# Kernel tuning notes

Measured on AMD Instinct MI355X. Metric: run time of the kernel, lower is better.

## Reference

```python
import jax, jax.numpy as jnp
import numpy as np

EPS_FEAT = 1e-4   # stabilizer eps inside favorp_projection
EPS_DEN = 0.01    # clamp_min eps for the attention denominator


def favorp_projection(data, projection_matrix, is_query):
    # data: [b, h, n, d]; projection_matrix: [h, m, d]
    d = data.shape[-1]
    data_normalizer = d ** (-0.25)
    ratio = projection_matrix.shape[1] ** (-0.5)
    data_dash = jnp.einsum('bhnd,hmd->bhnm', data_normalizer * data, projection_matrix)
    diag_data = (jnp.sum(data * data, axis=-1) * 0.5 * data_normalizer * data_normalizer)[..., None]
    if is_query:
        stabilizer = jax.lax.stop_gradient(jnp.max(data_dash, axis=-1, keepdims=True))
    else:
        stabilizer = jax.lax.stop_gradient(jnp.max(data_dash, axis=(-1, -2), keepdims=True))
    return ratio * jnp.exp(data_dash - diag_data - stabilizer) + EPS_FEAT


def setup_inputs() -> dict:
    key = jax.random.key(0)
    ks = jax.random.split(key, 12)
    N, B, E, H, D, M = 4096, 4, 1024, 16, 64, 64
    s = E ** -0.5
    return {
        'query': jax.random.normal(ks[0], (N, B, E), jnp.float32),
        'key': jax.random.normal(ks[1], (N, B, E), jnp.float32),
        'value': jax.random.normal(ks[2], (N, B, E), jnp.float32),
        'Wq': jax.random.normal(ks[3], (E, E), jnp.float32) * s,
        'bq': jax.random.normal(ks[4], (E,), jnp.float32) * 0.02,
        'Wk': jax.random.normal(ks[5], (E, E), jnp.float32) * s,
        'bk': jax.random.normal(ks[6], (E,), jnp.float32) * 0.02,
        'Wv': jax.random.normal(ks[7], (E, E), jnp.float32) * s,
        'bv': jax.random.normal(ks[8], (E,), jnp.float32) * 0.02,
        'Wo': jax.random.normal(ks[9], (E, E), jnp.float32) * s,
        'bo': jax.random.normal(ks[10], (E,), jnp.float32) * 0.02,
        'proj': jax.random.normal(ks[11], (H, M, D), jnp.float32),
    }


def reference(query, key, value, Wq, bq, Wk, bk, Wv, bv, Wo, bo, proj):
    H = proj.shape[0]
    # [n, b, e] -> [b, n, e]
    q_in = query.transpose(1, 0, 2)
    k_in = key.transpose(1, 0, 2)
    v_in = value.transpose(1, 0, 2)
    B, N, E = q_in.shape
    D = E // H

    def lin(x, W, b):
        return jnp.einsum('bne,fe->bnf', x, W) + b

    def split_heads(x):  # [b, n, e] -> [b, h, n, d]
        return x.reshape(B, N, H, D).transpose(0, 2, 1, 3)

    q = split_heads(lin(q_in, Wq, bq))
    k = split_heads(lin(k_in, Wk, bk))
    v = split_heads(lin(v_in, Wv, bv))

    q_prime = favorp_projection(q, proj, is_query=True)   # [b, h, n, m]
    k_prime = favorp_projection(k, proj, is_query=False)  # [b, h, n, m]

    # non-causal linear attention: O(n * m * d)
    kv = jnp.einsum('bhnm,bhnd->bhmd', k_prime, v)
    qkv = jnp.einsum('bhnm,bhmd->bhnd', q_prime, kv)
    normalizer = jnp.einsum('bhnm,bhm->bhn', q_prime, k_prime.sum(axis=2))
    output = qkv / jnp.maximum(normalizer[..., None], EPS_DEN)

    attn_output = output.transpose(0, 2, 1, 3).reshape(B, N, E)  # b h n d -> b n (h d)
    out = lin(attn_output, Wo, bo)
    return out.transpose(1, 0, 2)  # back to [n, b, e]
```

## Files before the change

### kernel.cpp

```cpp
#include <hip/hip_runtime.h>
#include <math.h>

#define B_   4
#define N_   4096
#define E_   1024
#define H_   16
#define BN_  (B_*N_)
#define BH_  (B_*H_)
#define SPLITK 8

#define NRM_C   0.35355339059327373f
#define DIAG_C  0.0625f
#define RATIO_C 0.125f
#define EPSF    1e-4f
#define EPSD    0.01f

typedef __attribute__((ext_vector_type(8))) short bf16x8;
typedef __attribute__((ext_vector_type(4))) float f32x4;

__device__ __forceinline__ unsigned short f32_to_bf16(float x) {
    unsigned int u = __float_as_uint(x);
    unsigned int r = (u + 0x7fffu + ((u >> 16) & 1u)) >> 16;
    return (unsigned short)r;
}
__device__ __forceinline__ float bf16_to_f32(unsigned short h) {
    return __uint_as_float(((unsigned int)h) << 16);
}

__device__ __forceinline__ unsigned int pk_bf16(float a, float b) {
    unsigned int r;
    asm("v_cvt_pk_bf16_f32 %0, %1, %2" : "=v"(r) : "v"(a), "v"(b));
    return r;
}

__device__ __forceinline__ void f32x8_split(float4 fa, float4 fb, bf16x8& hi, bf16x8& lo) {
    unsigned int h0 = pk_bf16(fa.x, fa.y), h1 = pk_bf16(fa.z, fa.w);
    unsigned int h2 = pk_bf16(fb.x, fb.y), h3 = pk_bf16(fb.z, fb.w);
    float e0 = __uint_as_float(h0 << 16), e1 = __uint_as_float(h0 & 0xffff0000u);
    float e2 = __uint_as_float(h1 << 16), e3 = __uint_as_float(h1 & 0xffff0000u);
    float e4 = __uint_as_float(h2 << 16), e5 = __uint_as_float(h2 & 0xffff0000u);
    float e6 = __uint_as_float(h3 << 16), e7 = __uint_as_float(h3 & 0xffff0000u);
    unsigned int l0 = pk_bf16(fa.x - e0, fa.y - e1), l1 = pk_bf16(fa.z - e2, fa.w - e3);
    unsigned int l2 = pk_bf16(fb.x - e4, fb.y - e5), l3 = pk_bf16(fb.z - e6, fb.w - e7);
    union { unsigned int u[4]; bf16x8 v; } H, L;
    H.u[0] = h0; H.u[1] = h1; H.u[2] = h2; H.u[3] = h3;
    L.u[0] = l0; L.u[1] = l1; L.u[2] = l2; L.u[3] = l3;
    hi = H.v; lo = L.v;
}

__device__ __forceinline__ void atomicMaxF(float* addr, float v) {
    if (v >= 0.f) atomicMax((int*)addr, __float_as_int(v));
    else          atomicMin((unsigned int*)addr, __float_as_uint(v));
}

__global__ void init_stab(float* stab) {
    if (threadIdx.x < BH_) stab[threadIdx.x] = -INFINITY;
}

template<int IN_MODE>
__global__ __launch_bounds__(256) void convert_split(const float* __restrict__ src,
                                                     unsigned short* __restrict__ hi,
                                                     unsigned short* __restrict__ lo,
                                                     int total4)
{
    int i = blockIdx.x * 256 + threadIdx.x;
    const int stride = gridDim.x * 256;
    for (; i < total4; i += stride) {
        long e4 = (long)i * 4;
        const float* p;
        if (IN_MODE == 0) {
            long r = e4 >> 10; int e = (int)(e4 & 1023);
            int b = (int)(r >> 12), n = (int)(r & 4095);
            p = src + (((long)(n * B_ + b)) << 10) + e;
        } else {
            p = src + e4;
        }
        float4 v = *(const float4*)p;
        ushort4 h, l;
        h.x = f32_to_bf16(v.x); l.x = f32_to_bf16(v.x - bf16_to_f32(h.x));
        h.y = f32_to_bf16(v.y); l.y = f32_to_bf16(v.y - bf16_to_f32(h.y));
        h.z = f32_to_bf16(v.z); l.z = f32_to_bf16(v.z - bf16_to_f32(h.z));
        h.w = f32_to_bf16(v.w); l.w = f32_to_bf16(v.w - bf16_to_f32(h.w));
        *(ushort4*)(hi + e4) = h;
        *(ushort4*)(lo + e4) = l;
    }
}

__device__ __forceinline__ void gl_lds16(const unsigned short* g, unsigned short* l) {
    __builtin_amdgcn_global_load_lds((const __attribute__((address_space(1))) void*)g,
                                     (__attribute__((address_space(3))) void*)l, 16, 0, 0);
}

#define SMEM_DYN8 147456

template<int MODE>
__global__ __launch_bounds__(512, 2) void gemm8p(const unsigned short* __restrict__ Ahi,
                                                 const unsigned short* __restrict__ Alo,
                                                 const unsigned short* __restrict__ Bhi,
                                                 const unsigned short* __restrict__ Blo,
                                                 const float* __restrict__ bias,
                                                 float* __restrict__ Y)
{
    extern __shared__ char SMEM8[];
    unsigned short* U = (unsigned short*)SMEM8;
    const int t = threadIdx.x;
    const int w = t >> 6, lane = t & 63;
    const int row0 = blockIdx.x * 256, col0 = blockIdx.y * 128;
    const int wrow = (w >> 1) * 64, wcol = (w & 1) * 64;
    const int g = lane >> 4, rl = lane & 15;

    int gi0 = t, gi1 = 512 + t;
    int ar0 = gi0 >> 2, as0 = gi0 & 3;
    int ar1 = gi1 >> 2, as1 = gi1 & 3;
    const long aSrc0 = (long)(row0 + ar0) * E_ + ((as0 ^ (ar0 & 3)) << 3);
    const long aSrc1 = (long)(row0 + ar1) * E_ + ((as1 ^ (ar1 & 3)) << 3);
    const int aDst0 = (w * 64) * 8;
    const int aDst1 = (512 + w * 64) * 8;
    const long bSrc = (long)(col0 + (t >> 2)) * E_ + (((t & 3) ^ ((t >> 2) & 3)) << 3);
    const int bDst = (w * 64) * 8;

    f32x4 acc[4][4];
#pragma unroll
    for (int m = 0; m < 4; ++m)
#pragma unroll
        for (int n = 0; n < 4; ++n) acc[m][n] = (f32x4){0.f, 0.f, 0.f, 0.f};

#define STAGE_FULL(TILE, BUFI) {                                        \
        const int k0_ = (TILE) * 32;                                    \
        unsigned short* bu_ = U + (BUFI) * 24576;                       \
        gl_lds16(Ahi + aSrc0 + k0_, bu_ + aDst0);                       \
        gl_lds16(Ahi + aSrc1 + k0_, bu_ + aDst1);                       \
        gl_lds16(Alo + aSrc0 + k0_, bu_ + 8192 + aDst0);                \
        gl_lds16(Alo + aSrc1 + k0_, bu_ + 8192 + aDst1);                \
        gl_lds16(Bhi + bSrc + k0_, bu_ + 16384 + bDst);                 \
        gl_lds16(Blo + bSrc + k0_, bu_ + 20480 + bDst); }

    STAGE_FULL(0, 0);
    STAGE_FULL(1, 1);
    asm volatile("s_waitcnt vmcnt(6)" ::: "memory");
    __builtin_amdgcn_s_barrier();
    __builtin_amdgcn_sched_barrier(0);

    for (int tt = 0; tt < 32; ++tt) {
        const unsigned short* sb = U + (tt % 3) * 24576;
        unsigned short* ub = U + ((tt + 2) % 3) * 24576;
        const bool st = (tt + 2 < 32);
        const int k2 = (tt + 2) * 32;
        bf16x8 bhf[4], blf[4];

#pragma unroll
        for (int n = 0; n < 4; ++n) {
            int r = wcol + n * 16 + rl;
            int off = r * 32 + ((g ^ (r & 3)) << 3);
            bhf[n] = *(const bf16x8*)(sb + 16384 + off);
            blf[n] = *(const bf16x8*)(sb + 20480 + off);
        }
        {
            int r = wrow + rl;
            int off = r * 32 + ((g ^ (r & 3)) << 3);
            bf16x8 ah = *(const bf16x8*)(sb + off);
            bf16x8 al = *(const bf16x8*)(sb + 8192 + off);
            if (st) { gl_lds16(Ahi + aSrc0 + k2, ub + aDst0);
                      gl_lds16(Ahi + aSrc1 + k2, ub + aDst1); }
            asm volatile("s_waitcnt lgkmcnt(0)" ::: "memory");
            __builtin_amdgcn_sched_barrier(0);
            __builtin_amdgcn_s_setprio(1);
#pragma unroll
            for (int n = 0; n < 4; ++n)
                acc[0][n] = __builtin_amdgcn_mfma_f32_16x16x32_bf16(ah, bhf[n], acc[0][n], 0, 0, 0);
#pragma unroll
            for (int n = 0; n < 4; ++n)
                acc[0][n] = __builtin_amdgcn_mfma_f32_16x16x32_bf16(ah, blf[n], acc[0][n], 0, 0, 0);
#pragma unroll
            for (int n = 0; n < 4; ++n)
                acc[0][n] = __builtin_amdgcn_mfma_f32_16x16x32_bf16(al, bhf[n], acc[0][n], 0, 0, 0);
            __builtin_amdgcn_s_setprio(0);
        }
        __builtin_amdgcn_s_barrier();
        __builtin_amdgcn_sched_barrier(0);

        {
            int r = wrow + 16 + rl;
            int off = r * 32 + ((g ^ (r & 3)) << 3);
            bf16x8 ah = *(const bf16x8*)(sb + off);
            bf16x8 al = *(const bf16x8*)(sb + 8192 + off);
            if (st) { gl_lds16(Alo + aSrc0 + k2, ub + 8192 + aDst0);
                      gl_lds16(Alo + aSrc1 + k2, ub + 8192 + aDst1); }
            asm volatile("s_waitcnt lgkmcnt(0)" ::: "memory");
            __builtin_amdgcn_sched_barrier(0);
            __builtin_amdgcn_s_setprio(1);
#pragma unroll
            for (int n = 0; n < 4; ++n)
                acc[1][n] = __builtin_amdgcn_mfma_f32_16x16x32_bf16(ah, bhf[n], acc[1][n], 0, 0, 0);
#pragma unroll
            for (int n = 0; n < 4; ++n)
                acc[1][n] = __builtin_amdgcn_mfma_f32_16x16x32_bf16(ah, blf[n], acc[1][n], 0, 0, 0);
#pragma unroll
            for (int n = 0; n < 4; ++n)
                acc[1][n] = __builtin_amdgcn_mfma_f32_16x16x32_bf16(al, bhf[n], acc[1][n], 0, 0, 0);
            __builtin_amdgcn_s_setprio(0);
        }
        __builtin_amdgcn_s_barrier();
        __builtin_amdgcn_sched_barrier(0);

        {
            int r = wrow + 32 + rl;
            int off = r * 32 + ((g ^ (r & 3)) << 3);
            bf16x8 ah = *(const bf16x8*)(sb + off);
            bf16x8 al = *(const bf16x8*)(sb + 8192 + off);
            if (st) gl_lds16(Bhi + bSrc + k2, ub + 16384 + bDst);
            asm volatile("s_waitcnt lgkmcnt(0)" ::: "memory");
            __builtin_amdgcn_sched_barrier(0);
            __builtin_amdgcn_s_setprio(1);
#pragma unroll
            for (int n = 0; n < 4; ++n)
                acc[2][n] = __builtin_amdgcn_mfma_f32_16x16x32_bf16(ah, bhf[n], acc[2][n], 0, 0, 0);
#pragma unroll
            for (int n = 0; n < 4; ++n)
                acc[2][n] = __builtin_amdgcn_mfma_f32_16x16x32_bf16(ah, blf[n], acc[2][n], 0, 0, 0);
#pragma unroll
            for (int n = 0; n < 4; ++n)
                acc[2][n] = __builtin_amdgcn_mfma_f32_16x16x32_bf16(al, bhf[n], acc[2][n], 0, 0, 0);
            __builtin_amdgcn_s_setprio(0);
        }
        __builtin_amdgcn_s_barrier();
        __builtin_amdgcn_sched_barrier(0);

        {
            int r = wrow + 48 + rl;
            int off = r * 32 + ((g ^ (r & 3)) << 3);
            bf16x8 ah = *(const bf16x8*)(sb + off);
            bf16x8 al = *(const bf16x8*)(sb + 8192 + off);
            if (st) gl_lds16(Blo + bSrc + k2, ub + 20480 + bDst);
            asm volatile("s_waitcnt lgkmcnt(0)" ::: "memory");
            __builtin_amdgcn_sched_barrier(0);
            __builtin_amdgcn_s_setprio(1);
#pragma unroll
            for (int n = 0; n < 4; ++n)
                acc[3][n] = __builtin_amdgcn_mfma_f32_16x16x32_bf16(ah, bhf[n], acc[3][n], 0, 0, 0);
#pragma unroll
            for (int n = 0; n < 4; ++n)
                acc[3][n] = __builtin_amdgcn_mfma_f32_16x16x32_bf16(ah, blf[n], acc[3][n], 0, 0, 0);
#pragma unroll
            for (int n = 0; n < 4; ++n)
                acc[3][n] = __builtin_amdgcn_mfma_f32_16x16x32_bf16(al, bhf[n], acc[3][n], 0, 0, 0);
            __builtin_amdgcn_s_setprio(0);
        }
        if (tt < 31) {
            if (st) asm volatile("s_waitcnt vmcnt(6)" ::: "memory");
            else    asm volatile("s_waitcnt vmcnt(0)" ::: "memory");
            __builtin_amdgcn_s_barrier();
            __builtin_amdgcn_sched_barrier(0);
        }
    }
#undef STAGE_FULL

    float bv[4];
#pragma unroll
    for (int n = 0; n < 4; ++n) bv[n] = bias[col0 + wcol + n * 16 + rl];
#pragma unroll
    for (int m = 0; m < 4; ++m) {
        int rbase = row0 + wrow + m * 16 + g * 4;
#pragma unroll
        for (int n = 0; n < 4; ++n) {
            int c = col0 + wcol + n * 16 + rl;
#pragma unroll
            for (int q = 0; q < 4; ++q) {
                int r = rbase + q;
                float v = acc[m][n][q] + bv[n];
                long off;
                if (MODE == 0) off = (long)r * E_ + c;
                else { int b = r >> 12, nn = r & (N_ - 1); off = (long)(nn * B_ + b) * E_ + c; }
                Y[off] = v;
            }
        }
    }
}

#define SMEM_BYTES (4*64*68*4 + 2*4*64*4)

template<int MODE>
__global__ __launch_bounds__(256) void gemm_mfma(const unsigned short* __restrict__ Ahi,
                                                 const unsigned short* __restrict__ Alo,
                                                 const unsigned short* __restrict__ Bhi,
                                                 const unsigned short* __restrict__ Blo,
                                                 const float* __restrict__ bias,
                                                 float* __restrict__ Y,
                                                 float* __restrict__ stab,
                                                 const unsigned short* __restrict__ PShi,
                                                 const unsigned short* __restrict__ PSlo,
                                                 const unsigned short* __restrict__ kvThi,
                                                 const unsigned short* __restrict__ kvTlo,
                                                 const float* __restrict__ ksum,
                                                 unsigned short* __restrict__ AttnHi,
                                                 unsigned short* __restrict__ AttnLo)
{
    __shared__ __align__(16) char SMEM[SMEM_BYTES];
    unsigned short* smem = (unsigned short*)SMEM;
    const int t = threadIdx.x;
    const int w = t >> 6, lane = t & 63;
    const int row0 = blockIdx.x * 128, col0 = blockIdx.y * 128;
    const int wrow = (w >> 1) * 64, wcol = (w & 1) * 64;
    const int g = lane >> 4, rl = lane & 15;
    const int lr8 = lane >> 3, lc8 = lane & 7;

    const int sr = w * 32 + (lane >> 2);
    const int kswz = (((lane & 3) ^ ((lane >> 2) & 3)) << 3);
    const long aoff = (long)(row0 + sr) * E_ + kswz;
    const long boff = (long)(col0 + sr) * E_ + kswz;

    f32x4 acc[4][4];
#pragma unroll
    for (int m = 0; m < 4; ++m)
#pragma unroll
        for (int n = 0; n < 4; ++n) acc[m][n] = (f32x4){0.f, 0.f, 0.f, 0.f};

#define STAGE_STEP(KS, BUF)                                                          \
    {                                                                                \
        const int k0 = (KS) * 32;                                                    \
        unsigned short* d = smem + (BUF) * 16384 + w * 1024;                         \
        gl_lds16(Ahi + aoff + k0,             d);                                    \
        gl_lds16(Ahi + aoff + k0 + 16 * E_,   d + 512);                              \
        gl_lds16(Alo + aoff + k0,             d + 4096);                             \
        gl_lds16(Alo + aoff + k0 + 16 * E_,   d + 4096 + 512);                       \
        gl_lds16(Bhi + boff + k0,             d + 8192);                             \
        gl_lds16(Bhi + boff + k0 + 16 * E_,   d + 8192 + 512);                       \
        gl_lds16(Blo + boff + k0,             d + 12288);                            \
        gl_lds16(Blo + boff + k0 + 16 * E_,   d + 12288 + 512);                      \
    }

    STAGE_STEP(0, 0);

    for (int ks = 0; ks < 32; ++ks) {
        __syncthreads();
        if (ks + 1 < 32) STAGE_STEP(ks + 1, (ks + 1) & 1);
        const unsigned short* sb = smem + (ks & 1) * 16384;
        bf16x8 ah[4], al[4], bh[4], bl[4];
#pragma unroll
        for (int m = 0; m < 4; ++m) {
            int r = wrow + m * 16 + rl;
            int off = r * 32 + ((g ^ (r & 3)) << 3);
            ah[m] = *(const bf16x8*)(sb + off);
            al[m] = *(const bf16x8*)(sb + 4096 + off);
        }
#pragma unroll
        for (int n = 0; n < 4; ++n) {
            int r = wcol + n * 16 + rl;
            int off = r * 32 + ((g ^ (r & 3)) << 3);
            bh[n] = *(const bf16x8*)(sb + 8192 + off);
            bl[n] = *(const bf16x8*)(sb + 12288 + off);
        }
#pragma unroll
        for (int m = 0; m < 4; ++m)
#pragma unroll
            for (int n = 0; n < 4; ++n)
                acc[m][n] = __builtin_amdgcn_mfma_f32_16x16x32_bf16(ah[m], bh[n], acc[m][n], 0, 0, 0);
#pragma unroll
        for (int m = 0; m < 4; ++m)
#pragma unroll
            for (int n = 0; n < 4; ++n)
                acc[m][n] = __builtin_amdgcn_mfma_f32_16x16x32_bf16(ah[m], bl[n], acc[m][n], 0, 0, 0);
#pragma unroll
        for (int m = 0; m < 4; ++m)
#pragma unroll
            for (int n = 0; n < 4; ++n)
                acc[m][n] = __builtin_amdgcn_mfma_f32_16x16x32_bf16(al[m], bh[n], acc[m][n], 0, 0, 0);
    }
#undef STAGE_STEP

    float bv[4];
#pragma unroll
    for (int n = 0; n < 4; ++n) bv[n] = bias[col0 + wcol + n * 16 + rl];

    __syncthreads();
    float* accF  = (float*)SMEM + w * (64 * 68);
    float* diagL = (float*)(SMEM + 4*64*68*4) + w * 64;
    float* rnmL  = (float*)(SMEM + 4*64*68*4) + 256 + w * 64;
    const int b_idx = row0 >> 12;
    const int hg = (col0 >> 6) + (w & 1);
    const int bh_i = b_idx * H_ + hg;

    bf16x8 pbh[8], pbl[8];
#pragma unroll
    for (int n = 0; n < 4; ++n)
#pragma unroll
        for (int kk = 0; kk < 2; ++kk) {
            long po = (long)hg * 4096 + (n*16 + rl) * 64 + kk*32 + g*8;
            pbh[n*2+kk] = *(const bf16x8*)(PShi + po);
            pbl[n*2+kk] = *(const bf16x8*)(PSlo + po);
        }

#pragma unroll
    for (int m = 0; m < 4; ++m)
#pragma unroll
        for (int n = 0; n < 4; ++n)
#pragma unroll
            for (int q = 0; q < 4; ++q)
                accF[(m*16 + g*4 + q) * 68 + n*16 + rl] = acc[m][n][q] + bv[n];
    {
        float s = 0.f;
#pragma unroll 16
        for (int d = 0; d < 64; ++d) { float x = accF[lane * 68 + d]; s = fmaf(x, x, s); }
        diagL[lane] = s * DIAG_C;
    }
    __syncthreads();

    float wavemax = -INFINITY;
#pragma unroll
    for (int mi = 0; mi < 4; ++mi) {
        bf16x8 dah[2], dal[2];
#pragma unroll
        for (int kk = 0; kk < 2; ++kk) {
            const float* src = &accF[(mi*16 + rl) * 68 + kk*32 + g*8];
            float4 f0 = *(const float4*)src, f1 = *(const float4*)(src + 4);
            f32x8_split(f0, f1, dah[kk], dal[kk]);
        }
        f32x4 dacc[4];
#pragma unroll
        for (int n = 0; n < 4; ++n) dacc[n] = (f32x4){0.f,0.f,0.f,0.f};
#pragma unroll
        for (int n = 0; n < 4; ++n)
#pragma unroll
            for (int kk = 0; kk < 2; ++kk) {
                dacc[n] = __builtin_amdgcn_mfma_f32_16x16x32_bf16(dah[kk], pbh[n*2+kk], dacc[n], 0, 0, 0);
                dacc[n] = __builtin_amdgcn_mfma_f32_16x16x32_bf16(dah[kk], pbl[n*2+kk], dacc[n], 0, 0, 0);
                dacc[n] = __builtin_amdgcn_mfma_f32_16x16x32_bf16(dal[kk], pbh[n*2+kk], dacc[n], 0, 0, 0);
            }
        if (MODE == 2) {
#pragma unroll
            for (int n = 0; n < 4; ++n)
#pragma unroll
                for (int q = 0; q < 4; ++q) {
                    float dsh = dacc[n][q] * NRM_C;
                    wavemax = fmaxf(wavemax, dsh);
                    int rloc = mi*16 + g*4 + q;
                    accF[rloc * 68 + n*16 + rl] = dsh - diagL[rloc];
                }
        } else {
            float rm0 = -INFINITY, rm1 = -INFINITY, rm2 = -INFINITY, rm3 = -INFINITY;
#pragma unroll
            for (int n = 0; n < 4; ++n) {
                rm0 = fmaxf(rm0, dacc[n][0]); rm1 = fmaxf(rm1, dacc[n][1]);
                rm2 = fmaxf(rm2, dacc[n][2]); rm3 = fmaxf(rm3, dacc[n][3]);
            }
#pragma unroll
            for (int off = 1; off < 16; off <<= 1) {
                rm0 = fmaxf(rm0, __shfl_xor(rm0, off));
                rm1 = fmaxf(rm1, __shfl_xor(rm1, off));
                rm2 = fmaxf(rm2, __shfl_xor(rm2, off));
                rm3 = fmaxf(rm3, __shfl_xor(rm3, off));
            }
            float rmq[4] = {rm0 * NRM_C, rm1 * NRM_C, rm2 * NRM_C, rm3 * NRM_C};
#pragma unroll
            for (int n = 0; n < 4; ++n)
#pragma unroll
                for (int q = 0; q < 4; ++q) {
                    int rloc = mi*16 + g*4 + q;
                    float qp = RATIO_C * expf(dacc[n][q] * NRM_C - diagL[rloc] - rmq[q]) + EPSF;
                    accF[rloc * 68 + n*16 + rl] = qp;
                }
        }
    }

    if (MODE == 2) {
#pragma unroll
        for (int off = 1; off < 64; off <<= 1) wavemax = fmaxf(wavemax, __shfl_xor(wavemax, off));
        if (lane == 0) atomicMaxF(&stab[bh_i], wavemax);
#pragma unroll
        for (int pass = 0; pass < 8; ++pass) {
            int rloc = pass * 8 + lr8;
            const float* sp = &accF[rloc * 68 + lc8 * 8];
            float4 f0 = *(const float4*)sp;
            float4 f1 = *(const float4*)(sp + 4);
            long off = (long)(row0 + wrow + rloc) * E_ + col0 + wcol + lc8 * 8;
            *(float4*)(Y + off) = f0;
            *(float4*)(Y + off + 4) = f1;
        }
        return;
    }

    {
        float s = 0.f;
        const float* kb = ksum + bh_i * 64;
#pragma unroll 16
        for (int m = 0; m < 64; ++m) s = fmaf(accF[lane * 68 + m], kb[m], s);
        rnmL[lane] = 1.f / fmaxf(s, EPSD);
    }
    bf16x8 kbh[8], kbl[8];
#pragma unroll
    for (int n = 0; n < 4; ++n)
#pragma unroll
        for (int kk = 0; kk < 2; ++kk) {
            long ko = (long)bh_i * 4096 + (n*16 + rl) * 64 + kk*32 + g*8;
            kbh[n*2+kk] = *(const bf16x8*)(kvThi + ko);
            kbl[n*2+kk] = *(const bf16x8*)(kvTlo + ko);
        }
    __syncthreads();
#pragma unroll
    for (int mi = 0; mi < 4; ++mi) {
        bf16x8 qah[2], qal[2];
#pragma unroll
        for (int kk = 0; kk < 2; ++kk) {
            const float* src = &accF[(mi*16 + rl) * 68 + kk*32 + g*8];
            float4 f0 = *(const float4*)src, f1 = *(const float4*)(src + 4);
            f32x8_split(f0, f1, qah[kk], qal[kk]);
        }
        f32x4 oacc[4];
#pragma unroll
        for (int n = 0; n < 4; ++n) oacc[n] = (f32x4){0.f,0.f,0.f,0.f};
#pragma unroll
        for (int n = 0; n < 4; ++n)
#pragma unroll
            for (int kk = 0; kk < 2; ++kk) {
                oacc[n] = __builtin_amdgcn_mfma_f32_16x16x32_bf16(qah[kk], kbh[n*2+kk], oacc[n], 0, 0, 0);
                oacc[n] = __builtin_amdgcn_mfma_f32_16x16x32_bf16(qah[kk], kbl[n*2+kk], oacc[n], 0, 0, 0);
                oacc[n] = __builtin_amdgcn_mfma_f32_16x16x32_bf16(qal[kk], kbh[n*2+kk], oacc[n], 0, 0, 0);
            }
#pragma unroll
        for (int n = 0; n < 4; ++n)
#pragma unroll
            for (int q = 0; q < 4; ++q) {
                int rloc = mi*16 + g*4 + q;
                accF[rloc * 68 + n*16 + rl] = oacc[n][q] * rnmL[rloc];
            }
    }
#pragma unroll
    for (int pass = 0; pass < 8; ++pass) {
        int rloc = pass * 8 + lr8;
        const float* sp = &accF[rloc * 68 + lc8 * 8];
        float4 f0 = *(const float4*)sp;
        float4 f1 = *(const float4*)(sp + 4);
        float v[8] = {f0.x,f0.y,f0.z,f0.w,f1.x,f1.y,f1.z,f1.w};
        unsigned int hu[4], lu[4];
#pragma unroll
        for (int j = 0; j < 4; ++j) {
            hu[j] = pk_bf16(v[2*j], v[2*j+1]);
            float ea = __uint_as_float(hu[j] << 16);
            float eb = __uint_as_float(hu[j] & 0xffff0000u);
            lu[j] = pk_bf16(v[2*j] - ea, v[2*j+1] - eb);
        }
        long off = (long)(row0 + wrow + rloc) * E_ + col0 + wcol + lc8 * 8;
        uint4 hv = {hu[0], hu[1], hu[2], hu[3]};
        uint4 lv = {lu[0], lu[1], lu[2], lu[3]};
        *(uint4*)(AttnHi + off) = hv;
        *(uint4*)(AttnLo + off) = lv;
    }
}

template<int IN_MODE, int OUT_MODE>
__global__ __launch_bounds__(256) void lin_gemm(const float* __restrict__ X,
                                                const float* __restrict__ W,
                                                const float* __restrict__ bias,
                                                float* __restrict__ Y)
{
    __shared__ float As[16][68];
    __shared__ float Ws[16][68];
    const int row0 = blockIdx.x * 64;
    const int col0 = blockIdx.y * 64;
    const int t  = threadIdx.x;
    const int lr = t >> 2;
    const int lk = (t & 3) * 4;
    const int ty = t >> 4, tx = t & 15;

    long arow;
    {
        int r = row0 + lr;
        if (IN_MODE == 0) { int b = r >> 12, n = r & (N_ - 1); arow = (long)(n * B_ + b) * E_; }
        else              { arow = (long)r * E_; }
    }
    const long wrow = (long)(col0 + lr) * E_;

    float acc[4][4] = {};
    for (int e0 = 0; e0 < E_; e0 += 16) {
        float4 av = *(const float4*)(X + arow + e0 + lk);
        float4 wv = *(const float4*)(W + wrow + e0 + lk);
        As[lk+0][lr] = av.x; As[lk+1][lr] = av.y; As[lk+2][lr] = av.z; As[lk+3][lr] = av.w;
        Ws[lk+0][lr] = wv.x; Ws[lk+1][lr] = wv.y; Ws[lk+2][lr] = wv.z; Ws[lk+3][lr] = wv.w;
        __syncthreads();
#pragma unroll
        for (int k = 0; k < 16; ++k) {
            float4 a = *(const float4*)&As[k][ty*4];
            float4 w = *(const float4*)&Ws[k][tx*4];
            float a_[4] = {a.x,a.y,a.z,a.w};
            float w_[4] = {w.x,w.y,w.z,w.w};
#pragma unroll
            for (int i = 0; i < 4; ++i)
#pragma unroll
                for (int j = 0; j < 4; ++j)
                    acc[i][j] = fmaf(a_[i], w_[j], acc[i][j]);
        }
        __syncthreads();
    }
    float4 bvv = *(const float4*)(bias + col0 + tx*4);
    float b_[4] = {bvv.x,bvv.y,bvv.z,bvv.w};
#pragma unroll
    for (int i = 0; i < 4; ++i) {
        int r = row0 + ty*4 + i;
        float4 o;
        o.x = acc[i][0] + b_[0]; o.y = acc[i][1] + b_[1];
        o.z = acc[i][2] + b_[2]; o.w = acc[i][3] + b_[3];
        long off;
        if (OUT_MODE == 0) off = (long)r * E_ + col0 + tx*4;
        else { int b = r >> 12, n = r & (N_ - 1); off = (long)(n * B_ + b) * E_ + col0 + tx*4; }
        *(float4*)(Y + off) = o;
    }
}

template<int IS_QUERY>
__global__ __launch_bounds__(256) void favorp_dash(float* __restrict__ Xh,
                                                   const float* __restrict__ proj,
                                                   float* __restrict__ stab)
{
    __shared__ float Xs[64][68];
    __shared__ float Ps[64][68];
    __shared__ float diag[64];
    __shared__ float red4[4];
    __shared__ float rowred[64][17];
    const int bh = blockIdx.x, b = bh >> 4, h = bh & 15;
    const int n0 = blockIdx.y * 64;
    const int t = threadIdx.x;
    const int r = t >> 2, c0 = (t & 3) * 16;
    const int ty = t >> 4, tx = t & 15;

    const float* xrow = Xh + (long)(b * N_ + n0 + r) * E_ + h * 64;
    const float* prow = proj + (long)(h * 64 + r) * 64;
#pragma unroll
    for (int c = 0; c < 4; ++c) {
        float4 v = *(const float4*)(xrow + c0 + c*4);
        Xs[c0+c*4+0][r] = v.x; Xs[c0+c*4+1][r] = v.y; Xs[c0+c*4+2][r] = v.z; Xs[c0+c*4+3][r] = v.w;
        float4 p = *(const float4*)(prow + c0 + c*4);
        Ps[c0+c*4+0][r] = p.x; Ps[c0+c*4+1][r] = p.y; Ps[c0+c*4+2][r] = p.z; Ps[c0+c*4+3][r] = p.w;
    }
    __syncthreads();
    if (t < 64) {
        float s = 0.f;
#pragma unroll 16
        for (int d = 0; d < 64; ++d) { float x = Xs[d][t]; s = fmaf(x, x, s); }
        diag[t] = s * DIAG_C;
    }
    __syncthreads();

    float acc[4][4] = {};
#pragma unroll 16
    for (int d = 0; d < 64; ++d) {
        float4 a = *(const float4*)&Xs[d][ty*4];
        float4 p = *(const float4*)&Ps[d][tx*4];
        float a_[4] = {a.x,a.y,a.z,a.w};
        float p_[4] = {p.x,p.y,p.z,p.w};
#pragma unroll
        for (int i = 0; i < 4; ++i)
#pragma unroll
            for (int j = 0; j < 4; ++j)
                acc[i][j] = fmaf(a_[i], p_[j], acc[i][j]);
    }
    float dash[4][4];
#pragma unroll
    for (int i = 0; i < 4; ++i)
#pragma unroll
        for (int j = 0; j < 4; ++j) dash[i][j] = acc[i][j] * NRM_C;

    if (IS_QUERY) {
#pragma unroll
        for (int i = 0; i < 4; ++i) {
            float m = fmaxf(fmaxf(dash[i][0], dash[i][1]), fmaxf(dash[i][2], dash[i][3]));
            rowred[ty*4+i][tx] = m;
        }
        __syncthreads();
#pragma unroll
        for (int i = 0; i < 4; ++i) {
            int row = ty*4 + i;
            float m = rowred[row][0];
#pragma unroll
            for (int jj = 1; jj < 16; ++jj) m = fmaxf(m, rowred[row][jj]);
            float dg = diag[row];
            float4 o;
            o.x = RATIO_C * expf(dash[i][0] - dg - m) + EPSF;
            o.y = RATIO_C * expf(dash[i][1] - dg - m) + EPSF;
            o.z = RATIO_C * expf(dash[i][2] - dg - m) + EPSF;
            o.w = RATIO_C * expf(dash[i][3] - dg - m) + EPSF;
            *(float4*)(Xh + (long)(b * N_ + n0 + row) * E_ + h * 64 + tx*4) = o;
        }
    } else {
        float lmax = dash[0][0];
#pragma unroll
        for (int i = 0; i < 4; ++i)
#pragma unroll
            for (int j = 0; j < 4; ++j) lmax = fmaxf(lmax, dash[i][j]);
#pragma unroll
        for (int i = 0; i < 4; ++i) {
            int row = ty*4 + i;
            float dg = diag[row];
            float4 o = { dash[i][0]-dg, dash[i][1]-dg, dash[i][2]-dg, dash[i][3]-dg };
            *(float4*)(Xh + (long)(b * N_ + n0 + row) * E_ + h * 64 + tx*4) = o;
        }
#pragma unroll
        for (int off = 32; off > 0; off >>= 1) lmax = fmaxf(lmax, __shfl_down(lmax, off));
        if ((t & 63) == 0) red4[t >> 6] = lmax;
        __syncthreads();
        if (t == 0)
            atomicMaxF(&stab[bh], fmaxf(fmaxf(red4[0], red4[1]), fmaxf(red4[2], red4[3])));
    }
}

__global__ __launch_bounds__(256) void kv_partial(const float* __restrict__ T1,
                                                  const float* __restrict__ V,
                                                  const float* __restrict__ stab,
                                                  float* __restrict__ kvp,
                                                  float* __restrict__ ksump)
{
    __shared__ float KPs[16][68];
    __shared__ float Vs[16][68];
    const int bh = blockIdx.x, chunk = blockIdx.y;
    const int b = bh >> 4, h = bh & 15;
    const int t = threadIdx.x;
    const int lr = t >> 4, lm = (t & 15) * 4;
    const int ty = t >> 4, tx = t & 15;
    const float stb = stab[bh];
    float acc[4][4] = {};
    float ks = 0.f;
    const int nbeg = chunk * (N_ / SPLITK), nend = nbeg + (N_ / SPLITK);
    for (int n0 = nbeg; n0 < nend; n0 += 16) {
        long rowoff = (long)(b * N_ + n0 + lr) * E_ + h * 64 + lm;
        float4 tv = *(const float4*)(T1 + rowoff);
        float4 vv = *(const float4*)(V + rowoff);
        KPs[lr][lm+0] = RATIO_C * expf(tv.x - stb) + EPSF;
        KPs[lr][lm+1] = RATIO_C * expf(tv.y - stb) + EPSF;
        KPs[lr][lm+2] = RATIO_C * expf(tv.z - stb) + EPSF;
        KPs[lr][lm+3] = RATIO_C * expf(tv.w - stb) + EPSF;
        *(float4*)&Vs[lr][lm] = vv;
        __syncthreads();
        if (t < 64) {
#pragma unroll
            for (int rr = 0; rr < 16; ++rr) ks += KPs[rr][t];
        }
#pragma unroll
        for (int k = 0; k < 16; ++k) {
            float4 a = *(const float4*)&KPs[k][ty*4];
            float4 v4 = *(const float4*)&Vs[k][tx*4];
            float a_[4] = {a.x,a.y,a.z,a.w};
            float v_[4] = {v4.x,v4.y,v4.z,v4.w};
#pragma unroll
            for (int i = 0; i < 4; ++i)
#pragma unroll
                for (int j = 0; j < 4; ++j)
                    acc[i][j] = fmaf(a_[i], v_[j], acc[i][j]);
        }
        __syncthreads();
    }
    const long kvbase = ((long)chunk * BH_ + bh) * 4096;
#pragma unroll
    for (int i = 0; i < 4; ++i) {
        float4 o = {acc[i][0], acc[i][1], acc[i][2], acc[i][3]};
        *(float4*)(kvp + kvbase + (ty*4+i) * 64 + tx*4) = o;
    }
    if (t < 64) ksump[((long)chunk * BH_ + bh) * 64 + t] = ks;
}

__global__ __launch_bounds__(256) void kv_reduce(const float* __restrict__ kvp,
                                                 const float* __restrict__ ksump,
                                                 float* __restrict__ kvM,
                                                 float* __restrict__ ksum,
                                                 unsigned short* __restrict__ kvThi,
                                                 unsigned short* __restrict__ kvTlo)
{
    int idx = blockIdx.x * 256 + threadIdx.x;
    if (idx < BH_ * 4096) {
        float s = 0.f;
#pragma unroll
        for (int c = 0; c < SPLITK; ++c) s += kvp[(long)c * BH_ * 4096 + idx];
        kvM[idx] = s;
        int bh = idx >> 12, md = idx & 4095, m = md >> 6, d = md & 63;
        unsigned short h16 = f32_to_bf16(s);
        long toff = (long)bh * 4096 + d * 64 + m;
        kvThi[toff] = h16;
        kvTlo[toff] = f32_to_bf16(s - bf16_to_f32(h16));
    } else {
        int j = idx - BH_ * 4096;
        if (j < BH_ * 64) {
            float s = 0.f;
#pragma unroll
            for (int c = 0; c < SPLITK; ++c) s += ksump[(long)c * BH_ * 64 + j];
            ksum[j] = s;
        }
    }
}

__global__ __launch_bounds__(256) void qkv_attn(const float* __restrict__ Qp,
                                                const float* __restrict__ kvM,
                                                const float* __restrict__ ksum,
                                                float* __restrict__ attn)
{
    __shared__ float QPs[64][68];
    __shared__ float kvs[64][68];
    __shared__ float ksums[64];
    __shared__ float rnorm[64];
    const int bh = blockIdx.x, b = bh >> 4, h = bh & 15;
    const int n0 = blockIdx.y * 64;
    const int t = threadIdx.x;
    const int r = t >> 2, c0 = (t & 3) * 16;
    const int ty = t >> 4, tx = t & 15;

#pragma unroll
    for (int c = 0; c < 4; ++c) {
        int idx = t * 16 + c * 4;
        float4 v = *(const float4*)(kvM + (long)bh * 4096 + idx);
        *(float4*)&kvs[idx >> 6][idx & 63] = v;
    }
    if (t < 64) ksums[t] = ksum[bh * 64 + t];
    const float* qrow = Qp + (long)(b * N_ + n0 + r) * E_ + h * 64;
#pragma unroll
    for (int c = 0; c < 4; ++c) {
        float4 v = *(const float4*)(qrow + c0 + c*4);
        QPs[c0+c*4+0][r] = v.x; QPs[c0+c*4+1][r] = v.y; QPs[c0+c*4+2][r] = v.z; QPs[c0+c*4+3][r] = v.w;
    }
    __syncthreads();
    if (t < 64) {
        float s = 0.f;
#pragma unroll 16
        for (int m = 0; m < 64; ++m) s = fmaf(QPs[m][t], ksums[m], s);
        rnorm[t] = 1.f / fmaxf(s, EPSD);
    }
    __syncthreads();
    float acc[4][4] = {};
#pragma unroll 16
    for (int m = 0; m < 64; ++m) {
        float4 a = *(const float4*)&QPs[m][ty*4];
        float4 v4 = *(const float4*)&kvs[m][tx*4];
        float a_[4] = {a.x,a.y,a.z,a.w};
        float v_[4] = {v4.x,v4.y,v4.z,v4.w};
#pragma unroll
        for (int i = 0; i < 4; ++i)
#pragma unroll
            for (int j = 0; j < 4; ++j)
                acc[i][j] = fmaf(a_[i], v_[j], acc[i][j]);
    }
#pragma unroll
    for (int i = 0; i < 4; ++i) {
        int row = ty*4 + i;
        float rn = rnorm[row];
        float4 o = {acc[i][0]*rn, acc[i][1]*rn, acc[i][2]*rn, acc[i][3]*rn};
        *(float4*)(attn + (long)(b * N_ + n0 + row) * E_ + h * 64 + tx*4) = o;
    }
}

extern "C" void kernel_launch(void* const* d_in, const int* in_sizes, int n_in,
                              void* d_out, int out_size, void* d_ws, size_t ws_size,
                              hipStream_t stream)
{
    const float* query = (const float*)d_in[0];
    const float* key   = (const float*)d_in[1];
    const float* value = (const float*)d_in[2];
    const float* Wq    = (const float*)d_in[3];
    const float* bq    = (const float*)d_in[4];
    const float* Wk    = (const float*)d_in[5];
    const float* bk    = (const float*)d_in[6];
    const float* Wv    = (const float*)d_in[7];
    const float* bv    = (const float*)d_in[8];
    const float* Wo    = (const float*)d_in[9];
    const float* bo    = (const float*)d_in[10];
    const float* proj  = (const float*)d_in[11];
    float* O = (float*)d_out;

    float* ws = (float*)d_ws;
    const size_t SZ = (size_t)BN_ * E_;
    float* A     = ws;
    float* kvp   = ws + SZ;
    float* ksump = kvp + (size_t)SPLITK * BH_ * 4096;
    float* kvM   = ksump + (size_t)SPLITK * BH_ * 64;
    float* ksum  = kvM + (size_t)BH_ * 4096;
    float* stab  = ksum + (size_t)BH_ * 64;
    unsigned short* kvThi = (unsigned short*)(stab + 64);
    unsigned short* kvTlo = kvThi + (size_t)BH_ * 4096;
    unsigned short* PShi  = kvTlo + (size_t)BH_ * 4096;
    unsigned short* PSlo  = PShi + 65536;
    const size_t EXTRA_F = (size_t)BH_ * 4096  + 65536 ;
    const size_t COMMON_F = SZ + (size_t)SPLITK * BH_ * 4096 + (size_t)SPLITK * BH_ * 64
                          + (size_t)BH_ * 4096 + (size_t)BH_ * 64 + 64 + EXTRA_F;
    unsigned short* Xhi = (unsigned short*)(ws + COMMON_F);
    unsigned short* Xlo = Xhi + SZ;
    unsigned short* Whi = Xlo + SZ;
    unsigned short* Wlo = Whi + (size_t)E_ * E_;
    const size_t NEED_FAST = (COMMON_F + SZ + (size_t)E_ * E_) * 4;

    dim3 gF(BH_, N_ / 64);
    dim3 gKV(BH_, SPLITK);
    const int nRed = (BH_ * 4096 + BH_ * 64) / 256;

    if (ws_size >= NEED_FAST) {
        dim3 gG(BN_ / 128, E_ / 128);
        dim3 gP(BN_ / 256, E_ / 128);
        const int X4 = (int)(SZ / 4), W4 = (E_ * E_) / 4;
        unsigned short* AttnHi = (unsigned short*)A;
        unsigned short* AttnLo = AttnHi + SZ;

        (void)hipFuncSetAttribute((const void*)&gemm8p<0>, hipFuncAttributeMaxDynamicSharedMemorySize, SMEM_DYN8);
        (void)hipFuncSetAttribute((const void*)&gemm8p<1>, hipFuncAttributeMaxDynamicSharedMemorySize, SMEM_DYN8);

        convert_split<1><<<64, 256, 0, stream>>>(proj, PShi, PSlo, 16384);
        init_stab<<<1, 64, 0, stream>>>(stab);
        convert_split<0><<<2048, 256, 0, stream>>>(key, Xhi, Xlo, X4);
        convert_split<1><<<1024, 256, 0, stream>>>(Wk, Whi, Wlo, W4);
        gemm_mfma<2><<<gG, 256, 0, stream>>>(Xhi, Xlo, Whi, Wlo, bk, O, stab,
                                             PShi, PSlo, nullptr, nullptr, nullptr, nullptr, nullptr);
        convert_split<0><<<2048, 256, 0, stream>>>(value, Xhi, Xlo, X4);
        convert_split<1><<<1024, 256, 0, stream>>>(Wv, Whi, Wlo, W4);
        gemm8p<0><<<gP, 512, SMEM_DYN8, stream>>>(Xhi, Xlo, Whi, Wlo, bv, A);
        kv_partial<<<gKV, 256, 0, stream>>>(O, A, stab, kvp, ksump);
        kv_reduce<<<nRed, 256, 0, stream>>>(kvp, ksump, kvM, ksum, kvThi, kvTlo);
        convert_split<0><<<2048, 256, 0, stream>>>(query, Xhi, Xlo, X4);
        convert_split<1><<<1024, 256, 0, stream>>>(Wq, Whi, Wlo, W4);
        gemm_mfma<3><<<gG, 256, 0, stream>>>(Xhi, Xlo, Whi, Wlo, bq, nullptr, nullptr,
                                             PShi, PSlo, kvThi, kvTlo, ksum, AttnHi, AttnLo);
        convert_split<1><<<1024, 256, 0, stream>>>(Wo, Whi, Wlo, W4);
        gemm8p<1><<<gP, 512, SMEM_DYN8, stream>>>(AttnHi, AttnLo, Whi, Wlo, bo, O);
    } else {
        dim3 gGemm(BN_ / 64, E_ / 64);
        lin_gemm<0,0><<<gGemm, 256, 0, stream>>>(key, Wk, bk, O);
        init_stab<<<1, 64, 0, stream>>>(stab);
        favorp_dash<0><<<gF, 256, 0, stream>>>(O, proj, stab);
        lin_gemm<0,0><<<gGemm, 256, 0, stream>>>(value, Wv, bv, A);
        kv_partial<<<gKV, 256, 0, stream>>>(O, A, stab, kvp, ksump);
        kv_reduce<<<nRed, 256, 0, stream>>>(kvp, ksump, kvM, ksum, kvThi, kvTlo);
        lin_gemm<0,0><<<gGemm, 256, 0, stream>>>(query, Wq, bq, O);
        favorp_dash<1><<<gF, 256, 0, stream>>>(O, proj, stab);
        qkv_attn<<<gF, 256, 0, stream>>>(O, kvM, ksum, A);
        lin_gemm<1,1><<<gGemm, 256, 0, stream>>>(A, Wo, bo, O);
    }
}
```

Baseline: 588.1 us.

## Move fused K/Q projection epilogues onto the 512-thread 256x128 pipelined GEMM

```diff
diff --git a/kernel.cpp b/kernel.cpp
--- a/kernel.cpp
+++ b/kernel.cpp
@@ -99,7 +99,15 @@
                                                  const unsigned short* __restrict__ Bhi,
                                                  const unsigned short* __restrict__ Blo,
                                                  const float* __restrict__ bias,
-                                                 float* __restrict__ Y)
+                                                 float* __restrict__ Y,
+                                                 float* __restrict__ stab,
+                                                 const unsigned short* __restrict__ PShi,
+                                                 const unsigned short* __restrict__ PSlo,
+                                                 const unsigned short* __restrict__ kvThi,
+                                                 const unsigned short* __restrict__ kvTlo,
+                                                 const float* __restrict__ ksum,
+                                                 unsigned short* __restrict__ AttnHi,
+                                                 unsigned short* __restrict__ AttnLo)
 {
     extern __shared__ char SMEM8[];
     unsigned short* U = (unsigned short*)SMEM8;
@@ -108,6 +116,7 @@
     const int row0 = blockIdx.x * 256, col0 = blockIdx.y * 128;
     const int wrow = (w >> 1) * 64, wcol = (w & 1) * 64;
     const int g = lane >> 4, rl = lane & 15;
+    const int lr8 = lane >> 3, lc8 = lane & 7;
 
     int gi0 = t, gi1 = 512 + t;
     int ar0 = gi0 >> 2, as0 = gi0 & 3;
@@ -258,124 +267,32 @@
     float bv[4];
 #pragma unroll
     for (int n = 0; n < 4; ++n) bv[n] = bias[col0 + wcol + n * 16 + rl];
-#pragma unroll
-    for (int m = 0; m < 4; ++m) {
-        int rbase = row0 + wrow + m * 16 + g * 4;
-#pragma unroll
-        for (int n = 0; n < 4; ++n) {
-            int c = col0 + wcol + n * 16 + rl;
-#pragma unroll
-            for (int q = 0; q < 4; ++q) {
-                int r = rbase + q;
-                float v = acc[m][n][q] + bv[n];
-                long off;
-                if (MODE == 0) off = (long)r * E_ + c;
-                else { int b = r >> 12, nn = r & (N_ - 1); off = (long)(nn * B_ + b) * E_ + c; }
-                Y[off] = v;
+
+    if (MODE <= 1) {
+#pragma unroll
+        for (int m = 0; m < 4; ++m) {
+            int rbase = row0 + wrow + m * 16 + g * 4;
+#pragma unroll
+            for (int n = 0; n < 4; ++n) {
+                int c = col0 + wcol + n * 16 + rl;
+#pragma unroll
+                for (int q = 0; q < 4; ++q) {
+                    int r = rbase + q;
+                    float v = acc[m][n][q] + bv[n];
+                    long off;
+                    if (MODE == 0) off = (long)r * E_ + c;
+                    else { int b = r >> 12, nn = r & (N_ - 1); off = (long)(nn * B_ + b) * E_ + c; }
+                    Y[off] = v;
+                }
             }
         }
-    }
-}
-
-#define SMEM_BYTES (4*64*68*4 + 2*4*64*4)
-
-template<int MODE>
-__global__ __launch_bounds__(256) void gemm_mfma(const unsigned short* __restrict__ Ahi,
-                                                 const unsigned short* __restrict__ Alo,
-                                                 const unsigned short* __restrict__ Bhi,
-                                                 const unsigned short* __restrict__ Blo,
-                                                 const float* __restrict__ bias,
-                                                 float* __restrict__ Y,
-                                                 float* __restrict__ stab,
-                                                 const unsigned short* __restrict__ PShi,
-                                                 const unsigned short* __restrict__ PSlo,
-                                                 const unsigned short* __restrict__ kvThi,
-                                                 const unsigned short* __restrict__ kvTlo,
-                                                 const float* __restrict__ ksum,
-                                                 unsigned short* __restrict__ AttnHi,
-                                                 unsigned short* __restrict__ AttnLo)
-{
-    __shared__ __align__(16) char SMEM[SMEM_BYTES];
-    unsigned short* smem = (unsigned short*)SMEM;
-    const int t = threadIdx.x;
-    const int w = t >> 6, lane = t & 63;
-    const int row0 = blockIdx.x * 128, col0 = blockIdx.y * 128;
-    const int wrow = (w >> 1) * 64, wcol = (w & 1) * 64;
-    const int g = lane >> 4, rl = lane & 15;
-    const int lr8 = lane >> 3, lc8 = lane & 7;
-
-    const int sr = w * 32 + (lane >> 2);
-    const int kswz = (((lane & 3) ^ ((lane >> 2) & 3)) << 3);
-    const long aoff = (long)(row0 + sr) * E_ + kswz;
-    const long boff = (long)(col0 + sr) * E_ + kswz;
-
-    f32x4 acc[4][4];
-#pragma unroll
-    for (int m = 0; m < 4; ++m)
-#pragma unroll
-        for (int n = 0; n < 4; ++n) acc[m][n] = (f32x4){0.f, 0.f, 0.f, 0.f};
-
-#define STAGE_STEP(KS, BUF)                                                          \
-    {                                                                                \
-        const int k0 = (KS) * 32;                                                    \
-        unsigned short* d = smem + (BUF) * 16384 + w * 1024;                         \
-        gl_lds16(Ahi + aoff + k0,             d);                                    \
-        gl_lds16(Ahi + aoff + k0 + 16 * E_,   d + 512);                              \
-        gl_lds16(Alo + aoff + k0,             d + 4096);                             \
-        gl_lds16(Alo + aoff + k0 + 16 * E_,   d + 4096 + 512);                       \
-        gl_lds16(Bhi + boff + k0,             d + 8192);                             \
-        gl_lds16(Bhi + boff + k0 + 16 * E_,   d + 8192 + 512);                       \
-        gl_lds16(Blo + boff + k0,             d + 12288);                            \
-        gl_lds16(Blo + boff + k0 + 16 * E_,   d + 12288 + 512);                      \
-    }
-
-    STAGE_STEP(0, 0);
-
-    for (int ks = 0; ks < 32; ++ks) {
-        __syncthreads();
-        if (ks + 1 < 32) STAGE_STEP(ks + 1, (ks + 1) & 1);
-        const unsigned short* sb = smem + (ks & 1) * 16384;
-        bf16x8 ah[4], al[4], bh[4], bl[4];
-#pragma unroll
-        for (int m = 0; m < 4; ++m) {
-            int r = wrow + m * 16 + rl;
-            int off = r * 32 + ((g ^ (r & 3)) << 3);
-            ah[m] = *(const bf16x8*)(sb + off);
-            al[m] = *(const bf16x8*)(sb + 4096 + off);
-        }
-#pragma unroll
-        for (int n = 0; n < 4; ++n) {
-            int r = wcol + n * 16 + rl;
-            int off = r * 32 + ((g ^ (r & 3)) << 3);
-            bh[n] = *(const bf16x8*)(sb + 8192 + off);
-            bl[n] = *(const bf16x8*)(sb + 12288 + off);
-        }
-#pragma unroll
-        for (int m = 0; m < 4; ++m)
-#pragma unroll
-            for (int n = 0; n < 4; ++n)
-                acc[m][n] = __builtin_amdgcn_mfma_f32_16x16x32_bf16(ah[m], bh[n], acc[m][n], 0, 0, 0);
-#pragma unroll
-        for (int m = 0; m < 4; ++m)
-#pragma unroll
-            for (int n = 0; n < 4; ++n)
-                acc[m][n] = __builtin_amdgcn_mfma_f32_16x16x32_bf16(ah[m], bl[n], acc[m][n], 0, 0, 0);
-#pragma unroll
-        for (int m = 0; m < 4; ++m)
-#pragma unroll
-            for (int n = 0; n < 4; ++n)
-                acc[m][n] = __builtin_amdgcn_mfma_f32_16x16x32_bf16(al[m], bh[n], acc[m][n], 0, 0, 0);
-    }
-#undef STAGE_STEP
-
-    float bv[4];
-#pragma unroll
-    for (int n = 0; n < 4; ++n) bv[n] = bias[col0 + wcol + n * 16 + rl];
+        return;
+    }
 
     __syncthreads();
-    float* accF  = (float*)SMEM + w * (64 * 68);
-    float* diagL = (float*)(SMEM + 4*64*68*4) + w * 64;
-    float* rnmL  = (float*)(SMEM + 4*64*68*4) + 256 + w * 64;
+    float* accF  = (float*)SMEM8 + w * (64 * 68);
+    float* diagL = (float*)(SMEM8 + 139264) + w * 64;
+    float* rnmL  = (float*)(SMEM8 + 139264 + 2048) + w * 64;
     const int b_idx = row0 >> 12;
     const int hg = (col0 >> 6) + (w & 1);
     const int bh_i = b_idx * H_ + hg;
@@ -887,7 +804,6 @@
     const int nRed = (BH_ * 4096 + BH_ * 64) / 256;
 
     if (ws_size >= NEED_FAST) {
-        dim3 gG(BN_ / 128, E_ / 128);
         dim3 gP(BN_ / 256, E_ / 128);
         const int X4 = (int)(SZ / 4), W4 = (E_ * E_) / 4;
         unsigned short* AttnHi = (unsigned short*)A;
@@ -895,24 +811,28 @@
 
         (void)hipFuncSetAttribute((const void*)&gemm8p<0>, hipFuncAttributeMaxDynamicSharedMemorySize, SMEM_DYN8);
         (void)hipFuncSetAttribute((const void*)&gemm8p<1>, hipFuncAttributeMaxDynamicSharedMemorySize, SMEM_DYN8);
+        (void)hipFuncSetAttribute((const void*)&gemm8p<2>, hipFuncAttributeMaxDynamicSharedMemorySize, SMEM_DYN8);
+        (void)hipFuncSetAttribute((const void*)&gemm8p<3>, hipFuncAttributeMaxDynamicSharedMemorySize, SMEM_DYN8);
 
         convert_split<1><<<64, 256, 0, stream>>>(proj, PShi, PSlo, 16384);
         init_stab<<<1, 64, 0, stream>>>(stab);
         convert_split<0><<<2048, 256, 0, stream>>>(key, Xhi, Xlo, X4);
         convert_split<1><<<1024, 256, 0, stream>>>(Wk, Whi, Wlo, W4);
-        gemm_mfma<2><<<gG, 256, 0, stream>>>(Xhi, Xlo, Whi, Wlo, bk, O, stab,
-                                             PShi, PSlo, nullptr, nullptr, nullptr, nullptr, nullptr);
+        gemm8p<2><<<gP, 512, SMEM_DYN8, stream>>>(Xhi, Xlo, Whi, Wlo, bk, O, stab,
+                                                  PShi, PSlo, nullptr, nullptr, nullptr, nullptr, nullptr);
         convert_split<0><<<2048, 256, 0, stream>>>(value, Xhi, Xlo, X4);
         convert_split<1><<<1024, 256, 0, stream>>>(Wv, Whi, Wlo, W4);
-        gemm8p<0><<<gP, 512, SMEM_DYN8, stream>>>(Xhi, Xlo, Whi, Wlo, bv, A);
+        gemm8p<0><<<gP, 512, SMEM_DYN8, stream>>>(Xhi, Xlo, Whi, Wlo, bv, A, nullptr,
+                                                  nullptr, nullptr, nullptr, nullptr, nullptr, nullptr, nullptr);
         kv_partial<<<gKV, 256, 0, stream>>>(O, A, stab, kvp, ksump);
         kv_reduce<<<nRed, 256, 0, stream>>>(kvp, ksump, kvM, ksum, kvThi, kvTlo);
         convert_split<0><<<2048, 256, 0, stream>>>(query, Xhi, Xlo, X4);
         convert_split<1><<<1024, 256, 0, stream>>>(Wq, Whi, Wlo, W4);
-        gemm_mfma<3><<<gG, 256, 0, stream>>>(Xhi, Xlo, Whi, Wlo, bq, nullptr, nullptr,
-                                             PShi, PSlo, kvThi, kvTlo, ksum, AttnHi, AttnLo);
+        gemm8p<3><<<gP, 512, SMEM_DYN8, stream>>>(Xhi, Xlo, Whi, Wlo, bq, nullptr, nullptr,
+                                                  PShi, PSlo, kvThi, kvTlo, ksum, AttnHi, AttnLo);
         convert_split<1><<<1024, 256, 0, stream>>>(Wo, Whi, Wlo, W4);
-        gemm8p<1><<<gP, 512, SMEM_DYN8, stream>>>(AttnHi, AttnLo, Whi, Wlo, bo, O);
+        gemm8p<1><<<gP, 512, SMEM_DYN8, stream>>>(AttnHi, AttnLo, Whi, Wlo, bo, O, nullptr,
+                                                  nullptr, nullptr, nullptr, nullptr, nullptr, nullptr, nullptr);
     } else {
         dim3 gGemm(BN_ / 64, E_ / 64);
         lin_gemm<0,0><<<gGemm, 256, 0, stream>>>(key, Wk, bk, O);
```

After: 582.2 us, median of 2. No clear change (-1.0%).
